# Performance work log

Hardware: AMD Instinct MI355X
Metric: run time of the kernel (lower is better)

Reference implementation:

```python
import jax, jax.numpy as jnp
import numpy as np

# Constants mirroring HomeostasisConfig defaults + STDP module constants
TARGET_RATE = 0.05
TRACE_DECAY = float(np.exp(-1.0 / 20.0))   # tau_plus = tau_minus = 20
ACT_DECAY   = 0.999                        # activity_decay / firing-rate EMA
BETA        = 0.9                          # LIF membrane leak
ETA_TH      = 0.001                        # threshold_adaptation_rate
MIN_W, MAX_W = -5.0, 5.0
MIN_TH, MAX_TH = 0.5, 2.0
LR          = 1.0                          # STDP learning_rate
TAG_THRESH  = 1e-3

B, T, IN, OUT = 128, 64, 2048, 2048


def setup_inputs() -> dict:
    key = jax.random.key(0)
    k1, k2 = jax.random.split(key, 2)
    # Bernoulli(0.1) rate-coded input spike trains (batch, time, in_features)
    x = (jax.random.uniform(k1, (B, T, IN)) < 0.1).astype(jnp.float32)
    W = jax.random.normal(k2, (OUT, IN), dtype=jnp.float32) * 0.1
    thresholds = jnp.ones((OUT,), dtype=jnp.float32)
    A_plus = jnp.asarray(0.01, dtype=jnp.float32)
    A_minus = jnp.asarray(0.012, dtype=jnp.float32)
    return {"x": x, "W": W, "thresholds": thresholds,
            "A_plus": A_plus, "A_minus": A_minus}


def _step(carry, x_t, A_plus, A_minus):
    v, Wc, th, pre_tr, post_tr, post_act, fr_ema, tags = carry
    # LIF membrane: leak + synaptic current, threshold, reset
    v = BETA * v + x_t @ Wc.T                      # (B, OUT)
    spk = (v >= th).astype(v.dtype)                # (B, OUT)
    v = v * (1.0 - spk)
    # trace / activity updates (batch-mean rates, as in update_traces)
    pre_rate = x_t.mean(axis=0)                    # (IN,)
    post_rate = spk.mean(axis=0)                   # (OUT,)
    pre_tr = TRACE_DECAY * pre_tr + pre_rate
    post_tr = TRACE_DECAY * post_tr + post_rate
    post_act = ACT_DECAY * post_act + (1.0 - ACT_DECAY) * post_rate
    # STDP: LTP/LTD outer products
    ltp = jnp.outer(post_rate, pre_tr) * jnp.abs(A_plus)
    ltd = jnp.outer(post_tr, pre_rate) * jnp.abs(A_minus)
    dw = ltp - ltd                                 # (OUT, IN)
    # metaplasticity factor
    meta = 1.0 / jnp.clip(post_act / TARGET_RATE, 0.5, 2.0)
    dw = dw * meta[:, None]
    # soft bounds
    w_range = MAX_W - MIN_W
    dw_b = jnp.where(dw > 0, dw * (MAX_W - Wc) / w_range,
                     dw * (Wc - MIN_W) / w_range)
    # synaptic tags
    tags = jnp.maximum(0.99 * tags, (jnp.abs(dw_b) > TAG_THRESH).astype(v.dtype))
    # apply STDP + clamp
    Wc = jnp.clip(Wc + LR * dw_b, MIN_W, MAX_W)
    # intrinsic plasticity: threshold homeostasis
    fr_ema = ACT_DECAY * fr_ema + (1.0 - ACT_DECAY) * post_rate
    th = jnp.clip(th * (1.0 + ETA_TH * (post_rate - TARGET_RATE)), MIN_TH, MAX_TH)
    return (v, Wc, th, pre_tr, post_tr, post_act, fr_ema, tags), spk


def reference(x, W, thresholds, A_plus, A_minus):
    b, t, n_in = x.shape
    n_out = W.shape[0]
    dt = x.dtype
    carry0 = (
        jnp.zeros((b, n_out), dt),                 # membrane potential
        W,                                         # weights
        thresholds,                                # per-neuron thresholds
        jnp.zeros((n_in,), dt),                    # pre trace
        jnp.zeros((n_out,), dt),                   # post trace
        jnp.full((n_out,), TARGET_RATE, dt),       # post activity EMA
        jnp.full((n_out,), TARGET_RATE, dt),       # firing-rate EMA
        jnp.zeros((n_out, n_in), dt),              # synaptic tags
    )
    step = lambda c, xt: _step(c, xt, A_plus, A_minus)
    _, spikes = jax.lax.scan(step, carry0, jnp.swapaxes(x, 0, 1))
    return jnp.swapaxes(spikes, 0, 1)              # (B, T, OUT)
```

## Files before the change

### kernel.cpp

```cpp
#include <hip/hip_runtime.h>
#include <cmath>

#define B_   128
#define T_   64
#define IN_  2048
#define OUT_ 2048
#define IDXSTRIDE 512
#define HALFSTRIDE 256
#define ZOFF 131072u

#define BETA_D   0.9
#define ACTDEC_D 0.999
#define ETA_TH_D 0.001
#define TARGET_D 0.05
#define MINW_D   (-5.0)
#define MAXW_D   (5.0)
#define MINTH_D  0.5
#define MAXTH_D  2.0

#define PART_OFF   131136
#define SMEM_BYTES 131200

__global__ __launch_bounds__(256) void k_rate(const float* __restrict__ x,
                                              double* __restrict__ pre_rate) {
    int t = blockIdx.x;
    int i = blockIdx.y * 256 + threadIdx.x;
    const float* xp = x + (size_t)t * IN_ + i;
    float s = 0.f;
    for (int b = 0; b < B_; ++b) s += xp[(size_t)b * T_ * IN_];
    pre_rate[(size_t)t * IN_ + i] = (double)s * (1.0 / 128.0);
}

__global__ __launch_bounds__(256) void k_scan(const double* __restrict__ pre_rate,
                                              double* __restrict__ pre_tr, double decay) {
    int i = blockIdx.x * 256 + threadIdx.x;
    double tr = 0.0;
    for (int t = 0; t < T_; ++t) {
        tr = decay * tr + pre_rate[(size_t)t * IN_ + i];
        pre_tr[(size_t)t * IN_ + i] = tr;
    }
}

__global__ __launch_bounds__(256) void k_build_idx(const float* __restrict__ x,
        unsigned* __restrict__ idx, int* __restrict__ cnt) {
    int row  = blockIdx.x * 4 + (threadIdx.x >> 6);
    int lane = threadIdx.x & 63;
    const float* xr = x + (size_t)row * IN_;
    unsigned* ip = idx + (size_t)row * IDXSTRIDE;
    unsigned long long below = (1ull << lane) - 1ull;
    int c = 0;
    for (int ch = 0; ch < IN_ / 64; ++ch) {
        int i = ch * 64 + lane;
        float vv = xr[i];
        unsigned long long m = __ballot(vv != 0.0f);
        if (vv != 0.0f) {
            int pos  = c + __popcll(m & below);
            int half = pos & 1, slot = pos >> 1;
            if (slot < HALFSTRIDE) ip[half * HALFSTRIDE + slot] = (unsigned)i << 6;
        }
        c += __popcll(m);
    }
    int ce = (c + 1) >> 1; if (ce > HALFSTRIDE) ce = HALFSTRIDE;
    int co = c >> 1;       if (co > HALFSTRIDE) co = HALFSTRIDE;
    int np = ((ce > co ? ce : co) + 7) & ~7;
    for (int p = ce + lane; p < np; p += 64) ip[p] = ZOFF;
    for (int p = co + lane; p < np; p += 64) ip[HALFSTRIDE + p] = ZOFF;
    if (lane == 0) cnt[row] = np;
}

#define GAT(r, A0, A1) do { \
    const double2 w_ = *(const double2*)(smem + ((r) ^ cx)); \
    A0 += w_.x; A1 += w_.y; } while (0)

__global__ __launch_bounds__(1024, 4) void k_main(
        const float* __restrict__ W, const float* __restrict__ thr,
        const float* __restrict__ Ap, const float* __restrict__ Am,
        const unsigned* __restrict__ idx, const int* __restrict__ cnt,
        const double* __restrict__ pre_rate, const double* __restrict__ pre_tr,
        float* __restrict__ out, double decay) {
    extern __shared__ char smem[];
    float* part = (float*)(smem + PART_OFF);

    const int tid  = threadIdx.x;
    const int s    = blockIdx.x;
    const int lane = tid & 63;
    const int h    = tid & 1;
    const int c2   = (tid >> 1) & 3;
    const int b    = tid >> 3;
    const unsigned cx = (unsigned)c2 << 4;

#pragma unroll
    for (int o = 0; o < 8; ++o) {
        const float* wr = W + (size_t)(s * 8 + o) * IN_;
        for (int i = tid; i < IN_; i += 1024) {
            *(double*)(smem + (((unsigned)i << 6) | ((unsigned)(o >> 1) << 4)
                               | ((unsigned)(o & 1) << 3))) = (double)wr[i];
        }
    }
    if (tid < 8)  ((double*)(smem + ZOFF))[tid] = 0.0;
    if (tid < 16) part[tid] = 0.0f;

    double th0 = (double)thr[s * 8 + c2 * 2];
    double th1 = (double)thr[s * 8 + c2 * 2 + 1];
    double ptr0 = 0.0, ptr1 = 0.0;
    double pact0 = TARGET_D, pact1 = TARGET_D;
    double vr0 = 0.0, vr1 = 0.0;
    const double apv = fabs((double)Ap[0]);
    const double amv = fabs((double)Am[0]);
    __syncthreads();

    const unsigned* ip0 = idx + (size_t)(b * T_) * IDXSTRIDE + h * HALFSTRIDE;
    int   n  = cnt[b * T_];
    uint4 q0 = *(const uint4*)(ip0);
    uint4 q1 = *(const uint4*)(ip0 + 4);

    for (int t = 0; t < T_; ++t) {
        const int pb = t & 1;
        const int row = b * T_ + t;
        const unsigned* ip = idx + (size_t)row * IDXSTRIDE + h * HALFSTRIDE;

        double a0 = 0.0, a1 = 0.0, e0 = 0.0, e1 = 0.0;
        if (n > 0) {
            int j = 0;
            for (;;) {
                uint4 qa = q0, qb = q1;
                int jn = j + 8;
                if (jn < n) {
                    q0 = *(const uint4*)(ip + jn);
                    q1 = *(const uint4*)(ip + jn + 4);
                }
                GAT(qa.x, a0, a1); GAT(qa.y, e0, e1);
                GAT(qa.z, a0, a1); GAT(qa.w, e0, e1);
                GAT(qb.x, a0, a1); GAT(qb.y, e0, e1);
                GAT(qb.z, a0, a1); GAT(qb.w, e0, e1);
                j = jn;
                if (j >= n) break;
            }
        }
        a0 += e0; a1 += e1;
        a0 += __shfl_xor(a0, 1);
        a1 += __shfl_xor(a1, 1);

        {
            int rown = row + ((t + 1 < T_) ? 1 : 0);
            const unsigned* ipn = idx + (size_t)rown * IDXSTRIDE + h * HALFSTRIDE;
            n  = cnt[rown];
            q0 = *(const uint4*)(ipn);
            q1 = *(const uint4*)(ipn + 4);
        }

        float s0 = 0.f, s1 = 0.f;
        if (h == 0) {
            double v0 = BETA_D * vr0 + a0;
            double v1 = BETA_D * vr1 + a1;
            s0 = (v0 >= th0) ? 1.0f : 0.0f;
            s1 = (v1 >= th1) ? 1.0f : 0.0f;
            *(float2*)(out + (size_t)row * OUT_ + s * 8 + c2 * 2) = make_float2(s0, s1);
            vr0 = (s0 != 0.0f) ? 0.0 : v0;
            vr1 = (s1 != 0.0f) ? 0.0 : v1;
        }

        if (t + 1 < T_) {
            float r0 = s0, r1 = s1;
            r0 += __shfl_xor(r0, 8);  r1 += __shfl_xor(r1, 8);
            r0 += __shfl_xor(r0, 16); r1 += __shfl_xor(r1, 16);
            r0 += __shfl_xor(r0, 32); r1 += __shfl_xor(r1, 32);
            if (lane < 8 && (lane & 1) == 0) {
                atomicAdd(&part[pb * 8 + c2 * 2], r0);
                atomicAdd(&part[pb * 8 + c2 * 2 + 1], r1);
            }
            if (tid < 8) part[(pb ^ 1) * 8 + tid] = 0.0f;
            __syncthreads();

            float cf0 = part[pb * 8 + c2 * 2];
            float cf1 = part[pb * 8 + c2 * 2 + 1];
            double prate0 = (double)cf0 * (1.0 / 128.0);
            double prate1 = (double)cf1 * (1.0 / 128.0);
            ptr0 = decay * ptr0 + prate0;
            ptr1 = decay * ptr1 + prate1;
            pact0 = ACTDEC_D * pact0 + (1.0 - ACTDEC_D) * prate0;
            pact1 = ACTDEC_D * pact1 + (1.0 - ACTDEC_D) * prate1;
            double r_ = pact0 / TARGET_D;
            r_ = r_ < 0.5 ? 0.5 : (r_ > 2.0 ? 2.0 : r_);
            double meta0 = 1.0 / r_;
            r_ = pact1 / TARGET_D;
            r_ = r_ < 0.5 ? 0.5 : (r_ > 2.0 ? 2.0 : r_);
            double meta1 = 1.0 / r_;
            double ca0 = apv * prate0 * meta0;
            double ca1 = apv * prate1 * meta1;
            double cb0 = amv * ptr0 * meta0;
            double cb1 = amv * ptr1 * meta1;
            double thv = th0 * (1.0 + ETA_TH_D * (prate0 - TARGET_D));
            th0 = thv < MINTH_D ? MINTH_D : (thv > MAXTH_D ? MAXTH_D : thv);
            thv = th1 * (1.0 + ETA_TH_D * (prate1 - TARGET_D));
            th1 = thv < MINTH_D ? MINTH_D : (thv > MAXTH_D ? MAXTH_D : thv);

            const double* prt = pre_tr   + (size_t)t * IN_;
            const double* prr = pre_rate + (size_t)t * IN_;
            const int b2 = (b << 1) | h;
#pragma unroll
            for (int k = 0; k < 8; ++k) {
                int i = k * 256 + b2;
                double p = prt[i], q = prr[i];
                double2* wp = (double2*)(smem + (((unsigned)i << 6) | cx));
                double2 w2 = *wp;
                double dw0 = ca0 * p - cb0 * q;
                double dw1 = ca1 * p - cb1 * q;
                double dwb0 = dw0 > 0.0 ? (dw0 * (MAXW_D - w2.x)) / 10.0
                                        : (dw0 * (w2.x - MINW_D)) / 10.0;
                double dwb1 = dw1 > 0.0 ? (dw1 * (MAXW_D - w2.y)) / 10.0
                                        : (dw1 * (w2.y - MINW_D)) / 10.0;
                double nw0 = w2.x + dwb0;
                nw0 = nw0 < MINW_D ? MINW_D : (nw0 > MAXW_D ? MAXW_D : nw0);
                double nw1 = w2.y + dwb1;
                nw1 = nw1 < MINW_D ? MINW_D : (nw1 > MAXW_D ? MAXW_D : nw1);
                *wp = make_double2(nw0, nw1);
            }
            __syncthreads();
        }
    }
}

extern "C" void kernel_launch(void* const* d_in, const int* in_sizes, int n_in,
                              void* d_out, int out_size, void* d_ws, size_t ws_size,
                              hipStream_t stream) {
    const float* x   = (const float*)d_in[0];
    const float* W   = (const float*)d_in[1];
    const float* thr = (const float*)d_in[2];
    const float* Ap  = (const float*)d_in[3];
    const float* Am  = (const float*)d_in[4];
    float* out = (float*)d_out;
    char* ws = (char*)d_ws;

    double* pre_rate = (double*)(ws);
    double* pre_tr   = (double*)(ws + 1048576);
    unsigned* idx    = (unsigned*)(ws + 2097152);
    int* cnt         = (int*)(ws + 2097152 + 16777216);

    double decay = std::exp(-1.0 / 20.0);

    (void)hipFuncSetAttribute((const void*)k_main,
                              hipFuncAttributeMaxDynamicSharedMemorySize, SMEM_BYTES);

    k_rate<<<dim3(T_, IN_ / 256), 256, 0, stream>>>(x, pre_rate);
    k_scan<<<IN_ / 256, 256, 0, stream>>>(pre_rate, pre_tr, decay);
    k_build_idx<<<(B_ * T_) / 4, 256, 0, stream>>>(x, idx, cnt);
    k_main<<<256, 1024, SMEM_BYTES, stream>>>(W, thr, Ap, Am, idx, cnt,
                                              pre_rate, pre_tr, out, decay);
}
```

Baseline: 835.0 us.

## Interleave pre trace/rate, prefetch them early, and widen gather unroll to 16

The scan kernel now writes the pre-trace and pre-rate as interleaved double2 pairs, so the main kernel fetches both with one vector load per element. Those loads are hoisted ahead of the spike/threshold logic so their latency overlaps the reductions. The sparse gather loop now handles 16 indices per iteration with padding to multiples of 16 and a minimum of 16, which removes the n>0 branch but adds extra zero-gathers for short rows.

Measured after the change: 844.8 us. About the same (+1.2%).

```diff
diff --git a/kernel.cpp b/kernel.cpp
--- a/kernel.cpp
+++ b/kernel.cpp
@@ -32,12 +32,13 @@
 }
 
 __global__ __launch_bounds__(256) void k_scan(const double* __restrict__ pre_rate,
-                                              double* __restrict__ pre_tr, double decay) {
+                                              double* __restrict__ prq, double decay) {
     int i = blockIdx.x * 256 + threadIdx.x;
     double tr = 0.0;
     for (int t = 0; t < T_; ++t) {
-        tr = decay * tr + pre_rate[(size_t)t * IN_ + i];
-        pre_tr[(size_t)t * IN_ + i] = tr;
+        double q = pre_rate[(size_t)t * IN_ + i];
+        tr = decay * tr + q;
+        *(double2*)&prq[((size_t)t * IN_ + i) * 2] = make_double2(tr, q);
     }
 }
 
@@ -62,7 +63,10 @@
     }
     int ce = (c + 1) >> 1; if (ce > HALFSTRIDE) ce = HALFSTRIDE;
     int co = c >> 1;       if (co > HALFSTRIDE) co = HALFSTRIDE;
-    int np = ((ce > co ? ce : co) + 7) & ~7;
+    int mx = ce > co ? ce : co;
+    int np = (mx + 15) & ~15;
+    if (np == 0) np = 16;
+    if (np > HALFSTRIDE) np = HALFSTRIDE;
     for (int p = ce + lane; p < np; p += 64) ip[p] = ZOFF;
     for (int p = co + lane; p < np; p += 64) ip[HALFSTRIDE + p] = ZOFF;
     if (lane == 0) cnt[row] = np;
@@ -76,8 +80,7 @@
         const float* __restrict__ W, const float* __restrict__ thr,
         const float* __restrict__ Ap, const float* __restrict__ Am,
         const unsigned* __restrict__ idx, const int* __restrict__ cnt,
-        const double* __restrict__ pre_rate, const double* __restrict__ pre_tr,
-        float* __restrict__ out, double decay) {
+        const double* __restrict__ prq, float* __restrict__ out, double decay) {
     extern __shared__ char smem[];
     float* part = (float*)(smem + PART_OFF);
 
@@ -107,12 +110,15 @@
     double vr0 = 0.0, vr1 = 0.0;
     const double apv = fabs((double)Ap[0]);
     const double amv = fabs((double)Am[0]);
+    const int b2 = (b << 1) | h;
     __syncthreads();
 
     const unsigned* ip0 = idx + (size_t)(b * T_) * IDXSTRIDE + h * HALFSTRIDE;
-    int   n  = cnt[b * T_];
-    uint4 q0 = *(const uint4*)(ip0);
-    uint4 q1 = *(const uint4*)(ip0 + 4);
+    int   n   = cnt[b * T_];
+    uint4 qa0 = *(const uint4*)(ip0);
+    uint4 qa1 = *(const uint4*)(ip0 + 4);
+    uint4 qb0 = *(const uint4*)(ip0 + 8);
+    uint4 qb1 = *(const uint4*)(ip0 + 12);
 
     for (int t = 0; t < T_; ++t) {
         const int pb = t & 1;
@@ -120,22 +126,26 @@
         const unsigned* ip = idx + (size_t)row * IDXSTRIDE + h * HALFSTRIDE;
 
         double a0 = 0.0, a1 = 0.0, e0 = 0.0, e1 = 0.0;
-        if (n > 0) {
-            int j = 0;
-            for (;;) {
-                uint4 qa = q0, qb = q1;
-                int jn = j + 8;
-                if (jn < n) {
-                    q0 = *(const uint4*)(ip + jn);
-                    q1 = *(const uint4*)(ip + jn + 4);
-                }
-                GAT(qa.x, a0, a1); GAT(qa.y, e0, e1);
-                GAT(qa.z, a0, a1); GAT(qa.w, e0, e1);
-                GAT(qb.x, a0, a1); GAT(qb.y, e0, e1);
-                GAT(qb.z, a0, a1); GAT(qb.w, e0, e1);
-                j = jn;
-                if (j >= n) break;
+        int j = 0;
+        for (;;) {
+            uint4 ca0 = qa0, ca1 = qa1, cb0 = qb0, cb1 = qb1;
+            int jn = j + 16;
+            if (jn < n) {
+                qa0 = *(const uint4*)(ip + jn);
+                qa1 = *(const uint4*)(ip + jn + 4);
+                qb0 = *(const uint4*)(ip + jn + 8);
+                qb1 = *(const uint4*)(ip + jn + 12);
             }
+            GAT(ca0.x, a0, a1); GAT(ca0.y, e0, e1);
+            GAT(ca0.z, a0, a1); GAT(ca0.w, e0, e1);
+            GAT(ca1.x, a0, a1); GAT(ca1.y, e0, e1);
+            GAT(ca1.z, a0, a1); GAT(ca1.w, e0, e1);
+            GAT(cb0.x, a0, a1); GAT(cb0.y, e0, e1);
+            GAT(cb0.z, a0, a1); GAT(cb0.w, e0, e1);
+            GAT(cb1.x, a0, a1); GAT(cb1.y, e0, e1);
+            GAT(cb1.z, a0, a1); GAT(cb1.w, e0, e1);
+            j = jn;
+            if (j >= n) break;
         }
         a0 += e0; a1 += e1;
         a0 += __shfl_xor(a0, 1);
@@ -144,9 +154,19 @@
         {
             int rown = row + ((t + 1 < T_) ? 1 : 0);
             const unsigned* ipn = idx + (size_t)rown * IDXSTRIDE + h * HALFSTRIDE;
-            n  = cnt[rown];
-            q0 = *(const uint4*)(ipn);
-            q1 = *(const uint4*)(ipn + 4);
+            n   = cnt[rown];
+            qa0 = *(const uint4*)(ipn);
+            qa1 = *(const uint4*)(ipn + 4);
+            qb0 = *(const uint4*)(ipn + 8);
+            qb1 = *(const uint4*)(ipn + 12);
+        }
+
+        double2 pq[8];
+        {
+            const double* pt = prq + ((size_t)t * IN_) * 2;
+#pragma unroll
+            for (int k = 0; k < 8; ++k)
+                pq[k] = *(const double2*)&pt[(k * 256 + b2) * 2];
         }
 
         float s0 = 0.f, s1 = 0.f;
@@ -195,13 +215,10 @@
             thv = th1 * (1.0 + ETA_TH_D * (prate1 - TARGET_D));
             th1 = thv < MINTH_D ? MINTH_D : (thv > MAXTH_D ? MAXTH_D : thv);
 
-            const double* prt = pre_tr   + (size_t)t * IN_;
-            const double* prr = pre_rate + (size_t)t * IN_;
-            const int b2 = (b << 1) | h;
 #pragma unroll
             for (int k = 0; k < 8; ++k) {
                 int i = k * 256 + b2;
-                double p = prt[i], q = prr[i];
+                double p = pq[k].x, q = pq[k].y;
                 double2* wp = (double2*)(smem + (((unsigned)i << 6) | cx));
                 double2 w2 = *wp;
                 double dw0 = ca0 * p - cb0 * q;
@@ -233,9 +250,9 @@
     char* ws = (char*)d_ws;
 
     double* pre_rate = (double*)(ws);
-    double* pre_tr   = (double*)(ws + 1048576);
-    unsigned* idx    = (unsigned*)(ws + 2097152);
-    int* cnt         = (int*)(ws + 2097152 + 16777216);
+    double* prq      = (double*)(ws + 1048576);
+    unsigned* idx    = (unsigned*)(ws + 1048576 + 2097152);
+    int* cnt         = (int*)(ws + 1048576 + 2097152 + 16777216);
 
     double decay = std::exp(-1.0 / 20.0);
 
@@ -243,8 +260,8 @@
                               hipFuncAttributeMaxDynamicSharedMemorySize, SMEM_BYTES);
 
     k_rate<<<dim3(T_, IN_ / 256), 256, 0, stream>>>(x, pre_rate);
-    k_scan<<<IN_ / 256, 256, 0, stream>>>(pre_rate, pre_tr, decay);
+    k_scan<<<IN_ / 256, 256, 0, stream>>>(pre_rate, prq, decay);
     k_build_idx<<<(B_ * T_) / 4, 256, 0, stream>>>(x, idx, cnt);
     k_main<<<256, 1024, SMEM_BYTES, stream>>>(W, thr, Ap, Am, idx, cnt,
-                                              pre_rate, pre_tr, out, decay);
-}
+                                              prq, out, decay);
+}
```

## Interleave pre trace/rate, prefetch before spike step, split index by lane parity

Applied to the files above, without the earlier changes.

The scan kernel now writes pre-trace and pre-rate interleaved as double2, and the main kernel loads them as 8 double2 values right after the gather, so their global latency overlaps the spike and reduction work instead of sitting inside the weight update loop. The index builder now splits nonzero inputs into even and odd halves by lane parity rather than by running position. Each half pads with a different zero slot, and the count is forced to at least 8 so the gather loop no longer needs an n>0 guard. This removes a branch and separate pre loads, at the cost of extra registers for the prefetched values and a gather over 8 padded entries when a row is empty.

Measured after the change: 808.2 us (median of 2 runs). 1.03x faster.

```diff
diff --git a/kernel.cpp b/kernel.cpp
--- a/kernel.cpp
+++ b/kernel.cpp
@@ -7,7 +7,8 @@
 #define OUT_ 2048
 #define IDXSTRIDE 512
 #define HALFSTRIDE 256
-#define ZOFF 131072u
+#define ZOFF  131072u
+#define ZOFF1 131136u
 
 #define BETA_D   0.9
 #define ACTDEC_D 0.999
@@ -18,8 +19,8 @@
 #define MINTH_D  0.5
 #define MAXTH_D  2.0
 
-#define PART_OFF   131136
-#define SMEM_BYTES 131200
+#define PART_OFF   131200
+#define SMEM_BYTES 131264
 
 __global__ __launch_bounds__(256) void k_rate(const float* __restrict__ x,
                                               double* __restrict__ pre_rate) {
@@ -32,12 +33,13 @@
 }
 
 __global__ __launch_bounds__(256) void k_scan(const double* __restrict__ pre_rate,
-                                              double* __restrict__ pre_tr, double decay) {
+                                              double* __restrict__ prq, double decay) {
     int i = blockIdx.x * 256 + threadIdx.x;
     double tr = 0.0;
     for (int t = 0; t < T_; ++t) {
-        tr = decay * tr + pre_rate[(size_t)t * IN_ + i];
-        pre_tr[(size_t)t * IN_ + i] = tr;
+        double q = pre_rate[(size_t)t * IN_ + i];
+        tr = decay * tr + q;
+        *(double2*)&prq[((size_t)t * IN_ + i) * 2] = make_double2(tr, q);
     }
 }
 
@@ -47,24 +49,34 @@
     int lane = threadIdx.x & 63;
     const float* xr = x + (size_t)row * IN_;
     unsigned* ip = idx + (size_t)row * IDXSTRIDE;
+    const unsigned long long EVEN = 0x5555555555555555ull;
     unsigned long long below = (1ull << lane) - 1ull;
-    int c = 0;
+    int ce = 0, co = 0;
     for (int ch = 0; ch < IN_ / 64; ++ch) {
         int i = ch * 64 + lane;
         float vv = xr[i];
         unsigned long long m = __ballot(vv != 0.0f);
+        unsigned long long me = m & EVEN, mo = m & ~EVEN;
         if (vv != 0.0f) {
-            int pos  = c + __popcll(m & below);
-            int half = pos & 1, slot = pos >> 1;
-            if (slot < HALFSTRIDE) ip[half * HALFSTRIDE + slot] = (unsigned)i << 6;
-        }
-        c += __popcll(m);
-    }
-    int ce = (c + 1) >> 1; if (ce > HALFSTRIDE) ce = HALFSTRIDE;
-    int co = c >> 1;       if (co > HALFSTRIDE) co = HALFSTRIDE;
-    int np = ((ce > co ? ce : co) + 7) & ~7;
+            if ((lane & 1) == 0) {
+                int pos = ce + __popcll(me & below);
+                if (pos < HALFSTRIDE) ip[pos] = (unsigned)i << 6;
+            } else {
+                int pos = co + __popcll(mo & below);
+                if (pos < HALFSTRIDE) ip[HALFSTRIDE + pos] = (unsigned)i << 6;
+            }
+        }
+        ce += __popcll(me);
+        co += __popcll(mo);
+    }
+    if (ce > HALFSTRIDE) ce = HALFSTRIDE;
+    if (co > HALFSTRIDE) co = HALFSTRIDE;
+    int mx = ce > co ? ce : co;
+    int np = (mx + 7) & ~7;
+    if (np == 0) np = 8;
+    if (np > HALFSTRIDE) np = HALFSTRIDE;
     for (int p = ce + lane; p < np; p += 64) ip[p] = ZOFF;
-    for (int p = co + lane; p < np; p += 64) ip[HALFSTRIDE + p] = ZOFF;
+    for (int p = co + lane; p < np; p += 64) ip[HALFSTRIDE + p] = ZOFF1;
     if (lane == 0) cnt[row] = np;
 }
 
@@ -76,8 +88,7 @@
         const float* __restrict__ W, const float* __restrict__ thr,
         const float* __restrict__ Ap, const float* __restrict__ Am,
         const unsigned* __restrict__ idx, const int* __restrict__ cnt,
-        const double* __restrict__ pre_rate, const double* __restrict__ pre_tr,
-        float* __restrict__ out, double decay) {
+        const double* __restrict__ prq, float* __restrict__ out, double decay) {
     extern __shared__ char smem[];
     float* part = (float*)(smem + PART_OFF);
 
@@ -97,7 +108,7 @@
                                | ((unsigned)(o & 1) << 3))) = (double)wr[i];
         }
     }
-    if (tid < 8)  ((double*)(smem + ZOFF))[tid] = 0.0;
+    if (tid < 16) ((double*)(smem + ZOFF))[tid] = 0.0;
     if (tid < 16) part[tid] = 0.0f;
 
     double th0 = (double)thr[s * 8 + c2 * 2];
@@ -107,6 +118,7 @@
     double vr0 = 0.0, vr1 = 0.0;
     const double apv = fabs((double)Ap[0]);
     const double amv = fabs((double)Am[0]);
+    const int b2 = (b << 1) | h;
     __syncthreads();
 
     const unsigned* ip0 = idx + (size_t)(b * T_) * IDXSTRIDE + h * HALFSTRIDE;
@@ -120,22 +132,20 @@
         const unsigned* ip = idx + (size_t)row * IDXSTRIDE + h * HALFSTRIDE;
 
         double a0 = 0.0, a1 = 0.0, e0 = 0.0, e1 = 0.0;
-        if (n > 0) {
-            int j = 0;
-            for (;;) {
-                uint4 qa = q0, qb = q1;
-                int jn = j + 8;
-                if (jn < n) {
-                    q0 = *(const uint4*)(ip + jn);
-                    q1 = *(const uint4*)(ip + jn + 4);
-                }
-                GAT(qa.x, a0, a1); GAT(qa.y, e0, e1);
-                GAT(qa.z, a0, a1); GAT(qa.w, e0, e1);
-                GAT(qb.x, a0, a1); GAT(qb.y, e0, e1);
-                GAT(qb.z, a0, a1); GAT(qb.w, e0, e1);
-                j = jn;
-                if (j >= n) break;
-            }
+        int j = 0;
+        for (;;) {
+            uint4 qa = q0, qb = q1;
+            int jn = j + 8;
+            if (jn < n) {
+                q0 = *(const uint4*)(ip + jn);
+                q1 = *(const uint4*)(ip + jn + 4);
+            }
+            GAT(qa.x, a0, a1); GAT(qa.y, e0, e1);
+            GAT(qa.z, a0, a1); GAT(qa.w, e0, e1);
+            GAT(qb.x, a0, a1); GAT(qb.y, e0, e1);
+            GAT(qb.z, a0, a1); GAT(qb.w, e0, e1);
+            j = jn;
+            if (j >= n) break;
         }
         a0 += e0; a1 += e1;
         a0 += __shfl_xor(a0, 1);
@@ -147,6 +157,14 @@
             n  = cnt[rown];
             q0 = *(const uint4*)(ipn);
             q1 = *(const uint4*)(ipn + 4);
+        }
+
+        double2 pq[8];
+        {
+            const double* pt = prq + ((size_t)t * IN_) * 2;
+#pragma unroll
+            for (int k = 0; k < 8; ++k)
+                pq[k] = *(const double2*)&pt[(k * 256 + b2) * 2];
         }
 
         float s0 = 0.f, s1 = 0.f;
@@ -195,13 +213,10 @@
             thv = th1 * (1.0 + ETA_TH_D * (prate1 - TARGET_D));
             th1 = thv < MINTH_D ? MINTH_D : (thv > MAXTH_D ? MAXTH_D : thv);
 
-            const double* prt = pre_tr   + (size_t)t * IN_;
-            const double* prr = pre_rate + (size_t)t * IN_;
-            const int b2 = (b << 1) | h;
 #pragma unroll
             for (int k = 0; k < 8; ++k) {
                 int i = k * 256 + b2;
-                double p = prt[i], q = prr[i];
+                double p = pq[k].x, q = pq[k].y;
                 double2* wp = (double2*)(smem + (((unsigned)i << 6) | cx));
                 double2 w2 = *wp;
                 double dw0 = ca0 * p - cb0 * q;
@@ -233,9 +248,9 @@
     char* ws = (char*)d_ws;
 
     double* pre_rate = (double*)(ws);
-    double* pre_tr   = (double*)(ws + 1048576);
-    unsigned* idx    = (unsigned*)(ws + 2097152);
-    int* cnt         = (int*)(ws + 2097152 + 16777216);
+    double* prq      = (double*)(ws + 1048576);
+    unsigned* idx    = (unsigned*)(ws + 1048576 + 2097152);
+    int* cnt         = (int*)(ws + 1048576 + 2097152 + 16777216);
 
     double decay = std::exp(-1.0 / 20.0);
 
@@ -243,8 +258,8 @@
                               hipFuncAttributeMaxDynamicSharedMemorySize, SMEM_BYTES);
 
     k_rate<<<dim3(T_, IN_ / 256), 256, 0, stream>>>(x, pre_rate);
-    k_scan<<<IN_ / 256, 256, 0, stream>>>(pre_rate, pre_tr, decay);
+    k_scan<<<IN_ / 256, 256, 0, stream>>>(pre_rate, prq, decay);
     k_build_idx<<<(B_ * T_) / 4, 256, 0, stream>>>(x, idx, cnt);
     k_main<<<256, 1024, SMEM_BYTES, stream>>>(W, thr, Ap, Am, idx, cnt,
-                                              pre_rate, pre_tr, out, decay);
-}
+                                              prq, out, decay);
+}
```
